# Kernel optimization log

Hardware: AMD Instinct MI355X
Metric: run time of the kernel (lower is better)

The kernel has to match this reference:

```python
import jax, jax.numpy as jnp
import numpy as np

DIM = 1024
HEADS = 16
DIM_HEAD = 64
INNER = HEADS * DIM_HEAD  # 1024
SCALE = DIM_HEAD ** -0.5


def setup_inputs() -> dict:
    key = jax.random.key(0)
    ks = jax.random.split(key, 5)
    b, n = 4, 2048
    x = jax.random.normal(ks[0], (b, n, DIM), dtype=jnp.float32)
    # nn.Linear weights, stored as (in, out) for x @ W
    w_q = jax.random.normal(ks[1], (DIM, INNER), dtype=jnp.float32) / np.sqrt(DIM)
    w_kv = jax.random.normal(ks[2], (DIM, 2 * DIM_HEAD), dtype=jnp.float32) / np.sqrt(DIM)
    w_out = jax.random.normal(ks[3], (INNER, DIM), dtype=jnp.float32) / np.sqrt(INNER)
    b_out = jax.random.normal(ks[4], (DIM,), dtype=jnp.float32) * 0.01
    return {"x": x, "w_q": w_q, "w_kv": w_kv, "w_out": w_out, "b_out": b_out}


def reference(x, w_q, w_kv, w_out, b_out):
    b, n, _ = x.shape
    # Q: [b, h, n, d]; K/V: single shared head [b, n, d]
    q = (x @ w_q).reshape(b, n, HEADS, DIM_HEAD).transpose(0, 2, 1, 3)
    kv = x @ w_kv  # [b, n, 2d]
    k, v = kv[..., :DIM_HEAD], kv[..., DIM_HEAD:]
    # scores: broadcast shared K across heads
    dots = jnp.einsum('bhnd,bmd->bhnm', q, k) * SCALE  # [b,h,n,n]
    attn = jax.nn.softmax(dots, axis=-1)
    out = jnp.einsum('bhnm,bmd->bhnd', attn, v)  # shared V across heads
    out = out.transpose(0, 2, 1, 3).reshape(b, n, INNER)
    return out @ w_out + b_out
```

## Files before the change

### kernel.cpp

```cpp
#include <hip/hip_runtime.h>
#include <hip/hip_bf16.h>
#include <stdint.h>

#define SEQ    2048
#define NBATCH 4
#define NHEADS 16
#define DHEAD  64
#define MODELD 1024
#define QKVN   1152
#define MROWS  (NBATCH*SEQ)
#define SCALE_LOG2E 0.1803368801111244f

typedef __bf16 bf16x8 __attribute__((ext_vector_type(8)));
typedef float  f32x4  __attribute__((ext_vector_type(4)));

typedef __attribute__((address_space(1))) void* as1_void_p;
typedef __attribute__((address_space(3))) void* as3_void_p;

__device__ __forceinline__ void gld_lds16(const void* g, void* l) {
  __builtin_amdgcn_global_load_lds((as1_void_p)(g), (as3_void_p)(l), 16, 0, 0);
}

__device__ __forceinline__ ushort f2bf(float f) {
  union { float f; uint32_t i; } t; t.f = f;
  uint32_t r = (t.i + 0x7fffu + ((t.i >> 16) & 1u)) >> 16;
  return (ushort)r;
}
__device__ __forceinline__ uint32_t pack_bf16(float a, float b) {
  union { __hip_bfloat162 h2; uint32_t u; } cv;
  cv.h2 = __float22bfloat162_rn(make_float2(a, b));
  return cv.u;
}

__device__ __forceinline__ void do_transpose(const float* __restrict__ src,
                                             ushort* __restrict__ dst,
                                             int R, int C, float scale,
                                             int gx, int gy, int tid) {
  __shared__ float tile[32][33];
  const int tx = tid & 31, ty = tid >> 5;
  const int c0 = gx * 32, r0 = gy * 32;
#pragma unroll
  for (int j = 0; j < 4; j++)
    tile[ty*4 + j][tx] = src[(size_t)(r0 + ty*4 + j) * C + c0 + tx];
  __syncthreads();
#pragma unroll
  for (int j = 0; j < 4; j++)
    dst[(size_t)(c0 + ty*4 + j) * R + r0 + tx] = f2bf(tile[tx][ty*4 + j] * scale);
}

__global__ __launch_bounds__(256)
void prep(const float* __restrict__ x, const float* __restrict__ w_q,
          const float* __restrict__ w_kv, const float* __restrict__ w_out,
          ushort* __restrict__ xb, ushort* __restrict__ wqkvT,
          ushort* __restrict__ woutT) {
  const int bid = blockIdx.x, tid = threadIdx.x;
  if (bid < 8192) {
    const size_t i = ((size_t)bid * 256 + tid) * 4;
    const float4 v = *(const float4*)(x + i);
    ushort4 o;
    o.x = f2bf(v.x); o.y = f2bf(v.y); o.z = f2bf(v.z); o.w = f2bf(v.w);
    *(ushort4*)(xb + i) = o;
  } else if (bid < 9216) {
    const int t = bid - 8192;
    do_transpose(w_q, wqkvT, MODELD, MODELD, SCALE_LOG2E, t & 31, t >> 5, tid);
  } else if (bid < 9344) {
    const int t = bid - 9216;
    do_transpose(w_kv, wqkvT + (size_t)MODELD * MODELD, MODELD, 128, 1.0f,
                 t & 3, t >> 2, tid);
  } else {
    const int t = bid - 9344;
    do_transpose(w_out, woutT, MODELD, MODELD, 1.0f, t & 31, t >> 5, tid);
  }
}

template <bool OUT_F32>
__global__ __launch_bounds__(256)
void gemm_bt(const ushort* __restrict__ A, const ushort* __restrict__ Bt,
             void* __restrict__ Cp, const float* __restrict__ bias,
             ushort* __restrict__ VT,
             int K, int lda, int ldb, int ldc) {
  __shared__ __attribute__((aligned(16))) ushort As[128*64];
  __shared__ __attribute__((aligned(16))) ushort Bs[128*64];
  const int tid = threadIdx.x;
  const int w = tid >> 6, lane = tid & 63;
  const int quad = lane >> 4, m16 = lane & 15;

  const int nwg = gridDim.x * gridDim.y;
  const int orig = blockIdx.y * gridDim.x + blockIdx.x;
  const int qq = nwg >> 3, rr = nwg & 7;
  const int xcd = orig & 7, loc = orig >> 3;
  const int L = (xcd < rr ? xcd * (qq + 1) : rr * (qq + 1) + (xcd - rr) * qq) + loc;
  const int bm0 = (L / gridDim.x) * 128, bn0 = (L % gridDim.x) * 128;

  f32x4 acc[4][4] = {};

  const int sr = lane >> 3;
  const int sg = ((lane & 7) ^ (sr & 7)) * 8;
  const ushort* Ag = A  + (size_t)(bm0 + w*32 + sr) * lda + sg;
  const ushort* Bg = Bt + (size_t)(bn0 + w*32 + sr) * ldb + sg;
  ushort* AsW = As + (w*32)*64;
  ushort* BsW = Bs + (w*32)*64;
  const int wm = (w >> 1) * 64, wn = (w & 1) * 64;

  for (int kb = 0; kb < K; kb += 64) {
#pragma unroll
    for (int c = 0; c < 4; c++) {
      gld_lds16(Ag + (size_t)(c*8)*lda + kb, AsW + c*8*64);
      gld_lds16(Bg + (size_t)(c*8)*ldb + kb, BsW + c*8*64);
    }
    __syncthreads();
#pragma unroll
    for (int kk = 0; kk < 2; kk++) {
      bf16x8 af[4], bfr[4];
      const int rg = ((kk*4 + quad) ^ (m16 & 7)) * 8;
#pragma unroll
      for (int mi = 0; mi < 4; mi++)
        af[mi] = *(const bf16x8*)(As + (wm + mi*16 + m16)*64 + rg);
#pragma unroll
      for (int ni = 0; ni < 4; ni++)
        bfr[ni] = *(const bf16x8*)(Bs + (wn + ni*16 + m16)*64 + rg);
#pragma unroll
      for (int mi = 0; mi < 4; mi++)
#pragma unroll
        for (int ni = 0; ni < 4; ni++)
          acc[mi][ni] = __builtin_amdgcn_mfma_f32_16x16x32_bf16(
              af[mi], bfr[ni], acc[mi][ni], 0, 0, 0);
    }
    __syncthreads();
  }

  const bool blockHasV = (VT != nullptr) && (bn0 + 128 > 1088);
#pragma unroll
  for (int ni = 0; ni < 4; ni++) {
    const int col = bn0 + wn + ni*16 + m16;
    const float bv = bias ? bias[col] : 0.0f;
#pragma unroll
    for (int mi = 0; mi < 4; mi++) {
#pragma unroll
      for (int r = 0; r < 4; r++) {
        const int row = bm0 + wm + mi*16 + quad*4 + r;
        const float v = acc[mi][ni][r] + bv;
        if (OUT_F32) ((float*)Cp)[(size_t)row*ldc + col] = v;
        else         ((ushort*)Cp)[(size_t)row*ldc + col] = f2bf(v);
        if (blockHasV && col >= 1088) {
          const int d = col - 1088, bb = row >> 11, n = row & 2047;
          VT[((size_t)bb * DHEAD + d) * SEQ + n] = f2bf(v);
        }
      }
    }
  }
}

__global__ __launch_bounds__(512, 2)
void mqa_attn(const ushort* __restrict__ qkv, const ushort* __restrict__ vT,
              ushort* __restrict__ attn_out) {
  __shared__ __attribute__((aligned(16))) ushort Ks[64*72];
  __shared__ __attribute__((aligned(16))) ushort Vs[80*72];
  __shared__ __attribute__((aligned(16))) ushort pbuf[8][32*72];

  const int tid = threadIdx.x;
  const int w = tid >> 6, lane = tid & 63;
  const int quad = lane >> 4, m16 = lane & 15;
  const int h = blockIdx.y * 2 + (w >> 2);
  const int b = blockIdx.z;
  const size_t rowbase = (size_t)b * SEQ;
  const int q0 = blockIdx.x * 128 + (w & 3) * 32;
  const ushort* vTb = vT + (size_t)b * DHEAD * SEQ;
  ushort* pb = pbuf[w];

  for (int i = tid; i < 16*72; i += 512)
    Vs[64*72 + i] = (i < 72) ? (ushort)0x3F80 : (ushort)0;

  const int srow = tid >> 3, scol = (tid & 7) * 8;
  const ushort* kgbase = qkv + (rowbase + srow) * QKVN + 1024 + scol;
  const ushort* vgbase = vTb + (size_t)srow * SEQ + scol;

  bf16x8 qf[2][2];
#pragma unroll
  for (int qt = 0; qt < 2; qt++) {
    const ushort* qrow = qkv + (rowbase + q0 + qt*16 + m16) * QKVN + h * DHEAD;
    qf[qt][0] = *(const bf16x8*)(qrow + quad*8);
    qf[qt][1] = *(const bf16x8*)(qrow + 32 + quad*8);
  }

  f32x4 o[2][4] = {};
  f32x4 o4[2]   = {};

  uint4 kreg = *(const uint4*)(kgbase);
  uint4 vreg = *(const uint4*)(vgbase);

  for (int kv0 = 0; kv0 < SEQ; kv0 += 64) {
    __syncthreads();
    *(uint4*)(Ks + srow*72 + scol) = kreg;
    *(uint4*)(Vs + srow*72 + scol) = vreg;
    __syncthreads();

    const int kvn = (kv0 + 64) & (SEQ - 1);
    kreg = *(const uint4*)(kgbase + (size_t)kvn * QKVN);
    vreg = *(const uint4*)(vgbase + kvn);

#pragma unroll
    for (int kh = 0; kh < 2; kh++) {
#pragma unroll
      for (int t2 = 0; t2 < 2; t2++) {
        const int t = kh*2 + t2;
        const bf16x8 kf0 = *(const bf16x8*)(Ks + (t*16 + m16)*72 + quad*8);
        const bf16x8 kf1 = *(const bf16x8*)(Ks + (t*16 + m16)*72 + 32 + quad*8);
#pragma unroll
        for (int qt = 0; qt < 2; qt++) {
          f32x4 s = {};
          s = __builtin_amdgcn_mfma_f32_16x16x32_bf16(kf0, qf[qt][0], s, 0, 0, 0);
          s = __builtin_amdgcn_mfma_f32_16x16x32_bf16(kf1, qf[qt][1], s, 0, 0, 0);
          float p[4];
#pragma unroll
          for (int r = 0; r < 4; r++)
            p[r] = __builtin_amdgcn_exp2f(s[r]);
          *(uint2*)(pb + (qt*16 + m16)*72 + kh*32 + t2*16 + quad*4) =
              make_uint2(pack_bf16(p[0], p[1]), pack_bf16(p[2], p[3]));
        }
      }
    }
    asm volatile("s_waitcnt lgkmcnt(0)" ::: "memory");

#pragma unroll
    for (int kh = 0; kh < 2; kh++) {
      bf16x8 pf[2], vf[4], vf4;
#pragma unroll
      for (int qt = 0; qt < 2; qt++)
        pf[qt] = *(const bf16x8*)(pb + (qt*16 + m16)*72 + kh*32 + quad*8);
#pragma unroll
      for (int dt = 0; dt < 4; dt++)
        vf[dt] = *(const bf16x8*)(Vs + (dt*16 + m16)*72 + kh*32 + quad*8);
      vf4 = *(const bf16x8*)(Vs + (64 + m16)*72 + kh*32 + quad*8);
      __builtin_amdgcn_s_setprio(1);
#pragma unroll
      for (int qt = 0; qt < 2; qt++) {
#pragma unroll
        for (int dt = 0; dt < 4; dt++)
          o[qt][dt] = __builtin_amdgcn_mfma_f32_16x16x32_bf16(vf[dt], pf[qt], o[qt][dt], 0, 0, 0);
        o4[qt] = __builtin_amdgcn_mfma_f32_16x16x32_bf16(vf4, pf[qt], o4[qt], 0, 0, 0);
      }
      __builtin_amdgcn_s_setprio(0);
    }
  }

#pragma unroll
  for (int qt = 0; qt < 2; qt++) {
    const float l = __shfl(o4[qt][0], m16, 64);
    const float inv = 1.0f / l;
    const size_t row = rowbase + q0 + qt*16 + m16;
#pragma unroll
    for (int dt = 0; dt < 4; dt++) {
      ushort4 st;
      st.x = f2bf(o[qt][dt][0] * inv);
      st.y = f2bf(o[qt][dt][1] * inv);
      st.z = f2bf(o[qt][dt][2] * inv);
      st.w = f2bf(o[qt][dt][3] * inv);
      *(ushort4*)(attn_out + row*MODELD + h*DHEAD + dt*16 + quad*4) = st;
    }
  }
}

extern "C" void kernel_launch(void* const* d_in, const int* in_sizes, int n_in,
                              void* d_out, int out_size, void* d_ws, size_t ws_size,
                              hipStream_t stream) {
  const float* x     = (const float*)d_in[0];
  const float* w_q   = (const float*)d_in[1];
  const float* w_kv  = (const float*)d_in[2];
  const float* w_out = (const float*)d_in[3];
  const float* b_out = (const float*)d_in[4];

  ushort* wqkvT = (ushort*)d_ws;
  ushort* woutT = wqkvT + (size_t)QKVN * MODELD;
  ushort* xb    = woutT + (size_t)MODELD * MODELD;
  ushort* qkv   = xb    + (size_t)MROWS * MODELD;
  ushort* attn  = qkv   + (size_t)MROWS * QKVN;
  ushort* vTb   = attn  + (size_t)MROWS * MODELD;

  prep<<<10368, 256, 0, stream>>>(x, w_q, w_kv, w_out, xb, wqkvT, woutT);

  gemm_bt<false><<<dim3(QKVN/128, MROWS/128), 256, 0, stream>>>(
      xb, wqkvT, (void*)qkv, nullptr, vTb, MODELD, MODELD, MODELD, QKVN);

  mqa_attn<<<dim3(SEQ/128, NHEADS/2, NBATCH), 512, 0, stream>>>(qkv, vTb, attn);

  gemm_bt<true><<<dim3(MODELD/128, MROWS/128), 256, 0, stream>>>(
      attn, woutT, d_out, b_out, nullptr, MODELD, MODELD, MODELD, MODELD);
}
```

Before: 235.1 us.

## Rewrite projection GEMMs with 128x256 tiles and 4-stage async LDS pipeline

Replaces the 128x128 single-buffered GEMM with a 512-thread 128x256 tile kernel. It uses a 4-deep ring of K=32 LDS stages filled by global_load_lds, with explicit vmcnt waits and barriers so loads overlap MFMA work. It also adds s_setprio around MFMA bursts and clamps B rows for the ragged 1152-wide QKV output. This removes the per-iteration load-then-compute stall and raises per-block reuse, but K is hardcoded to 1024 and the unswizzled 32-wide LDS rows may cause bank conflicts.

```diff
diff --git a/kernel.cpp b/kernel.cpp
--- a/kernel.cpp
+++ b/kernel.cpp
@@ -74,75 +74,102 @@
 }
 
 template <bool OUT_F32>
-__global__ __launch_bounds__(256)
-void gemm_bt(const ushort* __restrict__ A, const ushort* __restrict__ Bt,
-             void* __restrict__ Cp, const float* __restrict__ bias,
-             ushort* __restrict__ VT,
-             int K, int lda, int ldb, int ldc) {
-  __shared__ __attribute__((aligned(16))) ushort As[128*64];
-  __shared__ __attribute__((aligned(16))) ushort Bs[128*64];
+__global__ __launch_bounds__(512, 1)
+void gemm_bt2(const ushort* __restrict__ A, const ushort* __restrict__ Bt,
+              void* __restrict__ Cp, const float* __restrict__ bias,
+              ushort* __restrict__ VT,
+              int lda, int ldb, int ldc, int nB) {
+  __shared__ __attribute__((aligned(16))) ushort As[4][128*32];
+  __shared__ __attribute__((aligned(16))) ushort Bs[4][256*32];
   const int tid = threadIdx.x;
   const int w = tid >> 6, lane = tid & 63;
   const int quad = lane >> 4, m16 = lane & 15;
+  const int wr = w >> 2, wc = w & 3;
 
   const int nwg = gridDim.x * gridDim.y;
   const int orig = blockIdx.y * gridDim.x + blockIdx.x;
   const int qq = nwg >> 3, rr = nwg & 7;
   const int xcd = orig & 7, loc = orig >> 3;
   const int L = (xcd < rr ? xcd * (qq + 1) : rr * (qq + 1) + (xcd - rr) * qq) + loc;
-  const int bm0 = (L / gridDim.x) * 128, bn0 = (L % gridDim.x) * 128;
+  const int bm0 = (L / gridDim.x) * 128, bn0 = (L % gridDim.x) * 256;
 
   f32x4 acc[4][4] = {};
 
-  const int sr = lane >> 3;
-  const int sg = ((lane & 7) ^ (sr & 7)) * 8;
-  const ushort* Ag = A  + (size_t)(bm0 + w*32 + sr) * lda + sg;
-  const ushort* Bg = Bt + (size_t)(bn0 + w*32 + sr) * ldb + sg;
-  ushort* AsW = As + (w*32)*64;
-  ushort* BsW = Bs + (w*32)*64;
-  const int wm = (w >> 1) * 64, wn = (w & 1) * 64;
-
-  for (int kb = 0; kb < K; kb += 64) {
-#pragma unroll
-    for (int c = 0; c < 4; c++) {
-      gld_lds16(Ag + (size_t)(c*8)*lda + kb, AsW + c*8*64);
-      gld_lds16(Bg + (size_t)(c*8)*ldb + kb, BsW + c*8*64);
-    }
-    __syncthreads();
-#pragma unroll
-    for (int kk = 0; kk < 2; kk++) {
-      bf16x8 af[4], bfr[4];
-      const int rg = ((kk*4 + quad) ^ (m16 & 7)) * 8;
-#pragma unroll
-      for (int mi = 0; mi < 4; mi++)
-        af[mi] = *(const bf16x8*)(As + (wm + mi*16 + m16)*64 + rg);
-#pragma unroll
-      for (int ni = 0; ni < 4; ni++)
-        bfr[ni] = *(const bf16x8*)(Bs + (wn + ni*16 + m16)*64 + rg);
-#pragma unroll
-      for (int mi = 0; mi < 4; mi++)
-#pragma unroll
-        for (int ni = 0; ni < 4; ni++)
-          acc[mi][ni] = __builtin_amdgcn_mfma_f32_16x16x32_bf16(
-              af[mi], bfr[ni], acc[mi][ni], 0, 0, 0);
-    }
-    __syncthreads();
-  }
-
-  const bool blockHasV = (VT != nullptr) && (bn0 + 128 > 1088);
+  const int srA = tid >> 2, sgv = (tid & 3) * 8;
+  const ushort* Ag = A + (size_t)(bm0 + srA) * lda + sgv;
+  int brow0 = bn0 + srA;        if (brow0 >= nB) brow0 = nB - 1;
+  int brow1 = bn0 + 128 + srA;  if (brow1 >= nB) brow1 = nB - 1;
+  const ushort* Bg0 = Bt + (size_t)brow0 * ldb + sgv;
+  const ushort* Bg1 = Bt + (size_t)brow1 * ldb + sgv;
+
+#define STAGE(u) {                                              \
+    const int s_ = (u) & 3;                                     \
+    gld_lds16(Ag  + (u)*32, &As[s_][(w*16)*32]);                \
+    gld_lds16(Bg0 + (u)*32, &Bs[s_][(w*16)*32]);                \
+    gld_lds16(Bg1 + (u)*32, &Bs[s_][(128 + w*16)*32]); }
+
+#define BODY(t) {                                               \
+    const int s_ = (t) & 3;                                     \
+    const ushort* Asl = As[s_];                                 \
+    const ushort* Bsl = Bs[s_];                                 \
+    bf16x8 af[4], bf0[2], bf1[2];                               \
+    _Pragma("unroll")                                           \
+    for (int mi = 0; mi < 4; mi++)                              \
+      af[mi] = *(const bf16x8*)(Asl + (wr*64 + mi*16 + m16)*32 + quad*8); \
+    _Pragma("unroll")                                           \
+    for (int j = 0; j < 2; j++)                                 \
+      bf0[j] = *(const bf16x8*)(Bsl + (wc*64 + j*16 + m16)*32 + quad*8);  \
+    __builtin_amdgcn_s_setprio(1);                              \
+    _Pragma("unroll")                                           \
+    for (int mi = 0; mi < 4; mi++)                              \
+      _Pragma("unroll")                                         \
+      for (int j = 0; j < 2; j++)                               \
+        acc[mi][j] = __builtin_amdgcn_mfma_f32_16x16x32_bf16(af[mi], bf0[j], acc[mi][j], 0, 0, 0); \
+    __builtin_amdgcn_s_setprio(0);                              \
+    _Pragma("unroll")                                           \
+    for (int j = 0; j < 2; j++)                                 \
+      bf1[j] = *(const bf16x8*)(Bsl + (wc*64 + (2+j)*16 + m16)*32 + quad*8); \
+    __builtin_amdgcn_s_setprio(1);                              \
+    _Pragma("unroll")                                           \
+    for (int mi = 0; mi < 4; mi++)                              \
+      _Pragma("unroll")                                         \
+      for (int j = 0; j < 2; j++)                               \
+        acc[mi][2+j] = __builtin_amdgcn_mfma_f32_16x16x32_bf16(af[mi], bf1[j], acc[mi][2+j], 0, 0, 0); \
+    __builtin_amdgcn_s_setprio(0); }
+
+  STAGE(0); STAGE(1); STAGE(2);
+
+#pragma unroll 1
+  for (int t = 0; t < 30; ++t) {
+    asm volatile("s_waitcnt vmcnt(6)" ::: "memory");
+    asm volatile("s_barrier" ::: "memory");
+    if (t <= 28) STAGE(t + 3);
+    BODY(t);
+  }
+  asm volatile("s_waitcnt vmcnt(3)" ::: "memory");
+  asm volatile("s_barrier" ::: "memory");
+  BODY(30);
+  asm volatile("s_waitcnt vmcnt(0)" ::: "memory");
+  asm volatile("s_barrier" ::: "memory");
+  BODY(31);
+#undef STAGE
+#undef BODY
+
+  const bool hasV = (VT != nullptr) && (bn0 + 256 > 1088);
 #pragma unroll
   for (int ni = 0; ni < 4; ni++) {
-    const int col = bn0 + wn + ni*16 + m16;
+    const int col = bn0 + wc*64 + ni*16 + m16;
+    if (col >= nB) continue;
     const float bv = bias ? bias[col] : 0.0f;
 #pragma unroll
     for (int mi = 0; mi < 4; mi++) {
 #pragma unroll
       for (int r = 0; r < 4; r++) {
-        const int row = bm0 + wm + mi*16 + quad*4 + r;
+        const int row = bm0 + wr*64 + mi*16 + quad*4 + r;
         const float v = acc[mi][ni][r] + bv;
         if (OUT_F32) ((float*)Cp)[(size_t)row*ldc + col] = v;
         else         ((ushort*)Cp)[(size_t)row*ldc + col] = f2bf(v);
-        if (blockHasV && col >= 1088) {
+        if (hasV && col >= 1088) {
           const int d = col - 1088, bb = row >> 11, n = row & 2047;
           VT[((size_t)bb * DHEAD + d) * SEQ + n] = f2bf(v);
         }
@@ -279,11 +306,11 @@
 
   prep<<<10368, 256, 0, stream>>>(x, w_q, w_kv, w_out, xb, wqkvT, woutT);
 
-  gemm_bt<false><<<dim3(QKVN/128, MROWS/128), 256, 0, stream>>>(
-      xb, wqkvT, (void*)qkv, nullptr, vTb, MODELD, MODELD, MODELD, QKVN);
+  gemm_bt2<false><<<dim3(5, MROWS/128), 512, 0, stream>>>(
+      xb, wqkvT, (void*)qkv, nullptr, vTb, MODELD, MODELD, QKVN, QKVN);
 
   mqa_attn<<<dim3(SEQ/128, NHEADS/2, NBATCH), 512, 0, stream>>>(qkv, vTb, attn);
 
-  gemm_bt<true><<<dim3(MODELD/128, MROWS/128), 256, 0, stream>>>(
+  gemm_bt2<true><<<dim3(4, MROWS/128), 512, 0, stream>>>(
       attn, woutT, d_out, b_out, nullptr, MODELD, MODELD, MODELD, MODELD);
 }
```

Measured after the change: 254.6 us. +8.3%, slower.

## Double-buffer GEMM LDS tiles with K=32 stages and MFMA priority boost

Applied to the files above, without the earlier changes.

The GEMM main loop now stages K tiles of 32 instead of 64 into two LDS buffers. The next tile's global-to-LDS load is issued before computing on the current one, so memory latency overlaps with MFMA work and only one barrier is needed per iteration. It also drops the XOR swizzle on the LDS layout and raises wave priority around the MFMA block. The cost is twice as many loop iterations and barriers per K, and possible LDS bank conflicts from the unswizzled 64-byte rows.

```diff
diff --git a/kernel.cpp b/kernel.cpp
--- a/kernel.cpp
+++ b/kernel.cpp
@@ -79,8 +79,8 @@
              void* __restrict__ Cp, const float* __restrict__ bias,
              ushort* __restrict__ VT,
              int K, int lda, int ldb, int ldc) {
-  __shared__ __attribute__((aligned(16))) ushort As[128*64];
-  __shared__ __attribute__((aligned(16))) ushort Bs[128*64];
+  __shared__ __attribute__((aligned(16))) ushort As[2][128*32];
+  __shared__ __attribute__((aligned(16))) ushort Bs[2][128*32];
   const int tid = threadIdx.x;
   const int w = tid >> 6, lane = tid & 63;
   const int quad = lane >> 4, m16 = lane & 15;
@@ -94,40 +94,49 @@
 
   f32x4 acc[4][4] = {};
 
-  const int sr = lane >> 3;
-  const int sg = ((lane & 7) ^ (sr & 7)) * 8;
-  const ushort* Ag = A  + (size_t)(bm0 + w*32 + sr) * lda + sg;
-  const ushort* Bg = Bt + (size_t)(bn0 + w*32 + sr) * ldb + sg;
-  ushort* AsW = As + (w*32)*64;
-  ushort* BsW = Bs + (w*32)*64;
+  const int ar0 = w*32 + (lane >> 2);
+  const int ac0 = (lane & 3) * 8;
+  const ushort* Ag = A  + (size_t)(bm0 + ar0) * lda + ac0;
+  const ushort* Bg = Bt + (size_t)(bn0 + ar0) * ldb + ac0;
   const int wm = (w >> 1) * 64, wn = (w & 1) * 64;
 
-  for (int kb = 0; kb < K; kb += 64) {
-#pragma unroll
-    for (int c = 0; c < 4; c++) {
-      gld_lds16(Ag + (size_t)(c*8)*lda + kb, AsW + c*8*64);
-      gld_lds16(Bg + (size_t)(c*8)*ldb + kb, BsW + c*8*64);
-    }
+#define STAGE(t, buf) {                                         \
+    ushort* AsW = As[buf] + (w*32)*32;                          \
+    ushort* BsW = Bs[buf] + (w*32)*32;                          \
+    const int kb_ = (t) * 32;                                   \
+    gld_lds16(Ag + kb_,                  AsW);                  \
+    gld_lds16(Ag + (size_t)16*lda + kb_, AsW + 16*32);          \
+    gld_lds16(Bg + kb_,                  BsW);                  \
+    gld_lds16(Bg + (size_t)16*ldb + kb_, BsW + 16*32); }
+
+  STAGE(0, 0);
+  __syncthreads();
+  int cur = 0;
+  const int KT = K >> 5;
+#pragma unroll 1
+  for (int t = 0; t < KT; ++t) {
+    if (t + 1 < KT) STAGE(t + 1, cur ^ 1);
+    const ushort* Asl = As[cur];
+    const ushort* Bsl = Bs[cur];
+    bf16x8 af[4], bfr[4];
+#pragma unroll
+    for (int mi = 0; mi < 4; mi++)
+      af[mi] = *(const bf16x8*)(Asl + (wm + mi*16 + m16)*32 + quad*8);
+#pragma unroll
+    for (int ni = 0; ni < 4; ni++)
+      bfr[ni] = *(const bf16x8*)(Bsl + (wn + ni*16 + m16)*32 + quad*8);
+    __builtin_amdgcn_s_setprio(1);
+#pragma unroll
+    for (int mi = 0; mi < 4; mi++)
+#pragma unroll
+      for (int ni = 0; ni < 4; ni++)
+        acc[mi][ni] = __builtin_amdgcn_mfma_f32_16x16x32_bf16(
+            af[mi], bfr[ni], acc[mi][ni], 0, 0, 0);
+    __builtin_amdgcn_s_setprio(0);
     __syncthreads();
-#pragma unroll
-    for (int kk = 0; kk < 2; kk++) {
-      bf16x8 af[4], bfr[4];
-      const int rg = ((kk*4 + quad) ^ (m16 & 7)) * 8;
-#pragma unroll
-      for (int mi = 0; mi < 4; mi++)
-        af[mi] = *(const bf16x8*)(As + (wm + mi*16 + m16)*64 + rg);
-#pragma unroll
-      for (int ni = 0; ni < 4; ni++)
-        bfr[ni] = *(const bf16x8*)(Bs + (wn + ni*16 + m16)*64 + rg);
-#pragma unroll
-      for (int mi = 0; mi < 4; mi++)
-#pragma unroll
-        for (int ni = 0; ni < 4; ni++)
-          acc[mi][ni] = __builtin_amdgcn_mfma_f32_16x16x32_bf16(
-              af[mi], bfr[ni], acc[mi][ni], 0, 0, 0);
-    }
-    __syncthreads();
-  }
+    cur ^= 1;
+  }
+#undef STAGE
 
   const bool blockHasV = (VT != nullptr) && (bn0 + 128 > 1088);
 #pragma unroll
```

After: 247.6 us. 1.05x slower.
